# Performance work log

Measured on AMD Instinct MI355X. Metric: run time of the kernel, lower is better.

The kernel has to match this reference:

```python
import jax, jax.numpy as jnp
import numpy as np

B, S, D, H, E, K = 4, 1024, 1024, 4096, 8, 2


def setup_inputs() -> dict:
    key = jax.random.key(0)
    k1, k2, k3, k4 = jax.random.split(key, 4)
    x = jax.random.normal(k1, (B, S, D), dtype=jnp.float32)
    # expert params: two-layer MLP per expert, stacked along expert axis
    W1 = jax.random.normal(k2, (E, D, H), dtype=jnp.float32) * 0.02
    b1 = jnp.zeros((E, H), dtype=jnp.float32)
    W2 = jax.random.normal(k3, (E, H, D), dtype=jnp.float32) * 0.02
    b2 = jnp.zeros((E, D), dtype=jnp.float32)
    # hash-router assignments: k expert ids per token (stands in for HashRouter output)
    assign = jax.random.randint(k4, (B, S, K), 0, E, dtype=jnp.int64)
    return {"x": x, "W1": W1, "b1": b1, "W2": W2, "b2": b2, "assign": assign, "k": K}


def reference(x, W1, b1, W2, b2, assign, k):
    E_ = W1.shape[0]
    # mask[b,s,e] = 1 if expert e appears in assign[b,s,:] (matches (assign==idx).any(-1),
    # so a duplicated assignment contributes once, exactly like the torch loop)
    mask = (assign[..., None] == jnp.arange(E_)[None, None, None, :]).any(axis=-2)
    # run every token through every expert, then mask-combine (dense MoE reference)
    h = jax.nn.relu(jnp.einsum('bsd,edh->bseh', x, W1) + b1)      # [B,S,E,H]
    y = jnp.einsum('bseh,ehd->bsed', h, W2) + b2                  # [B,S,E,D]
    out = jnp.einsum('bsed,bse->bsd', y, mask.astype(x.dtype))
    return out / k
```

## Files before the change

kernel.cpp:

```cpp
#include <hip/hip_runtime.h>
#include <hip/hip_bf16.h>

#define DIM_D 1024
#define DIM_H 4096
#define NUM_E 8
#define NUM_TOK 4096
#define MAXROWS 8320

typedef __attribute__((ext_vector_type(8))) short short8;
typedef __attribute__((ext_vector_type(4))) float floatx4;

__device__ __forceinline__ unsigned short f2bf(float f) {
  union { float f; unsigned int u; } v; v.f = f;
  unsigned int r = v.u + 0x7fffu + ((v.u >> 16) & 1u);
  return (unsigned short)(r >> 16);
}

__device__ __forceinline__ void async_copy16(const void* g, void* l) {
  __builtin_amdgcn_global_load_lds(
      (__attribute__((address_space(1))) unsigned int*)(g),
      (__attribute__((address_space(3))) unsigned int*)(l), 16, 0, 0);
}


__global__ void route_count(const int* __restrict__ assign, int* __restrict__ counts) {
  int t = blockIdx.x * blockDim.x + threadIdx.x;
  if (t < NUM_TOK) {
    int e0 = assign[2 * t], e1 = assign[2 * t + 1];
    atomicAdd(&counts[e0], 1);
    if (e1 != e0) atomicAdd(&counts[e1], 1);
  }
}

__global__ void scan_k(const int* __restrict__ counts, int* __restrict__ offsets,
                       int* __restrict__ cursors) {
  if (threadIdx.x == 0 && blockIdx.x == 0) {
    int acc = 0;
    for (int e = 0; e < NUM_E; e++) {
      offsets[e] = acc; cursors[e] = acc; acc += counts[e];
    }
  }
}

__global__ void gather_k(const float* __restrict__ x, const int* __restrict__ assign,
                         int* __restrict__ cursors, int* __restrict__ tok2row,
                         unsigned short* __restrict__ Xg) {
  int t = blockIdx.x;
  __shared__ int sr[2];
  if (threadIdx.x == 0) {
    int e0 = assign[2 * t], e1 = assign[2 * t + 1];
    int r0 = atomicAdd(&cursors[e0], 1);
    int r1 = (e1 != e0) ? atomicAdd(&cursors[e1], 1) : -1;
    tok2row[2 * t] = r0; tok2row[2 * t + 1] = r1;
    sr[0] = r0; sr[1] = r1;
  }
  __syncthreads();
  int r0 = sr[0], r1 = sr[1];
  const float4* xv = (const float4*)(x + (size_t)t * DIM_D);
  float4 v0 = xv[threadIdx.x * 2];
  float4 v1 = xv[threadIdx.x * 2 + 1];
  unsigned short h[8];
  h[0] = f2bf(v0.x); h[1] = f2bf(v0.y); h[2] = f2bf(v0.z); h[3] = f2bf(v0.w);
  h[4] = f2bf(v1.x); h[5] = f2bf(v1.y); h[6] = f2bf(v1.z); h[7] = f2bf(v1.w);
  uint4 pack = *(uint4*)h;
  *(uint4*)(Xg + (size_t)r0 * DIM_D + threadIdx.x * 8) = pack;
  if (r1 >= 0)
    *(uint4*)(Xg + (size_t)r1 * DIM_D + threadIdx.x * 8) = pack;
}

__global__ void transpose_cvt(const float* __restrict__ in, unsigned short* __restrict__ outp,
                              int R, int C) {
  __shared__ float tile[64][65];
  int e = blockIdx.z;
  const float* ip = in + (size_t)e * R * C + (size_t)(blockIdx.y * 64) * C + blockIdx.x * 64;
  unsigned short* op = outp + (size_t)e * R * C + (size_t)(blockIdx.x * 64) * R + blockIdx.y * 64;
  int rr = threadIdx.x >> 4;
  int c4 = (threadIdx.x & 15) * 4;
#pragma unroll
  for (int i = 0; i < 4; i++) {
    int r = rr + i * 16;
    float4 v = *(const float4*)(ip + (size_t)r * C + c4);
    tile[r][c4 + 0] = v.x; tile[r][c4 + 1] = v.y;
    tile[r][c4 + 2] = v.z; tile[r][c4 + 3] = v.w;
  }
  __syncthreads();
  int r8 = (threadIdx.x & 7) * 8;
  int cbase = threadIdx.x >> 3;
#pragma unroll
  for (int it = 0; it < 2; it++) {
    int c = cbase + it * 32;
    unsigned short h[8];
#pragma unroll
    for (int j = 0; j < 8; j++) h[j] = f2bf(tile[r8 + j][c]);
    *(uint4*)(op + (size_t)c * R + r8) = *(const uint4*)h;
  }
}

template <int MODE>
__global__ __launch_bounds__(256) void moe_gemm(
    const unsigned short* __restrict__ A, const unsigned short* __restrict__ Bt,
    const float* __restrict__ bias, const int* __restrict__ counts,
    const int* __restrict__ offsets,
    unsigned short* __restrict__ Hout, float* __restrict__ Yout,
    int K, int N) {
  const int e = blockIdx.z;
  const int cnt = counts[e];
  int mt_, nt_;
  if (MODE == 0) {
    nt_ = (blockIdx.x & 7) | ((blockIdx.y & 3) << 3);
    mt_ = (blockIdx.x >> 3) | ((blockIdx.y >> 2) << 2);
  } else {
    nt_ = blockIdx.x; mt_ = blockIdx.y;
  }
  const int m0 = mt_ * 128;
  if (m0 >= cnt) return;
  const int n0 = nt_ * 128;
  const int rowbase = offsets[e];

  __shared__ unsigned short sh[2 * 128 * 64];
  unsigned short* As = sh;
  unsigned short* Bs = sh + 128 * 64;

  const int tid = threadIdx.x;
  const int w = tid >> 6;
  const int lane = tid & 63;
  const int l15 = lane & 15, l4 = lane >> 4;
  const int wm = w >> 1, wn = w & 1;
  const int lrow = lane >> 3, lslot = lane & 7;
  const int lchunk = lslot ^ lrow;

  const unsigned short* gA[4]; const unsigned short* gB[4];
  void* dA[4]; void* dB[4];
  const unsigned short* Bbase = Bt + (size_t)e * N * K;
#pragma unroll
  for (int p = 0; p < 4; p++) {
    int rw = p * 32 + w * 8;
    gA[p] = A + (size_t)(rowbase + m0 + rw + lrow) * K + lchunk * 8;
    gB[p] = Bbase + (size_t)(n0 + rw + lrow) * K + lchunk * 8;
    dA[p] = (char*)As + rw * 128;
    dB[p] = (char*)Bs + rw * 128;
  }

  floatx4 acc[4][4];
#pragma unroll
  for (int i = 0; i < 4; i++)
#pragma unroll
    for (int j = 0; j < 4; j++) acc[i][j] = (floatx4){0.f, 0.f, 0.f, 0.f};

  int arow[4], brow[4], sl[2];
  sl[0] = ((l4 + 0) ^ (l15 & 7)) * 8;
  sl[1] = ((l4 + 4) ^ (l15 & 7)) * 8;
#pragma unroll
  for (int mt = 0; mt < 4; mt++) arow[mt] = (wm * 64 + mt * 16 + l15) * 64;
#pragma unroll
  for (int nt = 0; nt < 4; nt++) brow[nt] = (wn * 64 + nt * 16 + l15) * 64;

  for (int k0 = 0; k0 < K; k0 += 64) {
    __syncthreads();
#pragma unroll
    for (int p = 0; p < 4; p++) async_copy16(gA[p], dA[p]);
#pragma unroll
    for (int p = 0; p < 4; p++) async_copy16(gB[p], dB[p]);
#pragma unroll
    for (int p = 0; p < 4; p++) { gA[p] += 64; gB[p] += 64; }
    __syncthreads();
#pragma unroll
    for (int s = 0; s < 2; s++) {
      short8 a[4], b[4];
#pragma unroll
      for (int mt = 0; mt < 4; mt++) a[mt] = *(const short8*)(As + arow[mt] + sl[s]);
#pragma unroll
      for (int nt = 0; nt < 4; nt++) b[nt] = *(const short8*)(Bs + brow[nt] + sl[s]);
#pragma unroll
      for (int mt = 0; mt < 4; mt++)
#pragma unroll
        for (int nt = 0; nt < 4; nt++)
          acc[mt][nt] = __builtin_amdgcn_mfma_f32_16x16x32_bf16(a[mt], b[nt], acc[mt][nt], 0, 0, 0);
    }
  }

  __syncthreads();
  float* sbuf = (float*)sh + w * 1088;
  const float* be = bias + (size_t)e * N + n0 + wn * 64;
#pragma unroll
  for (int mt = 0; mt < 4; mt++) {
#pragma unroll
    for (int nt = 0; nt < 4; nt++) {
      float bv = be[nt * 16 + l15];
#pragma unroll
      for (int r = 0; r < 4; r++) {
        float v = acc[mt][nt][r] + bv;
        if (MODE == 0) v = fmaxf(v, 0.f);
        sbuf[(l4 * 4 + r) * 68 + nt * 16 + l15] = v;
      }
    }
    __syncthreads();
#pragma unroll
    for (int pass = 0; pass < 4; pass++) {
      int row = pass * 4 + l4;
      int col4 = l15 * 4;
      int gm = m0 + wm * 64 + mt * 16 + row;
      float4 v = *(const float4*)&sbuf[row * 68 + col4];
      if (gm < cnt) {
        size_t off = (size_t)(rowbase + gm) * N + n0 + wn * 64 + col4;
        if (MODE == 0) {
          ushort4 h;
          h.x = f2bf(v.x); h.y = f2bf(v.y); h.z = f2bf(v.z); h.w = f2bf(v.w);
          *(ushort4*)(Hout + off) = h;
        } else {
          *(float4*)(Yout + off) = v;
        }
      }
    }
    __syncthreads();
  }
}

__global__ void combine_k(const float* __restrict__ Yg, const int* __restrict__ tok2row,
                          const int* __restrict__ kptr, float* __restrict__ out) {
  int t = blockIdx.x;
  int r0 = tok2row[2 * t], r1 = tok2row[2 * t + 1];
  float invk = 1.0f / (float)kptr[0];
  int d = threadIdx.x * 4;
  float4 v = *(const float4*)(Yg + (size_t)r0 * DIM_D + d);
  if (r1 >= 0) {
    float4 u = *(const float4*)(Yg + (size_t)r1 * DIM_D + d);
    v.x += u.x; v.y += u.y; v.z += u.z; v.w += u.w;
  }
  float4 o; o.x = v.x * invk; o.y = v.y * invk; o.z = v.z * invk; o.w = v.w * invk;
  *(float4*)(out + (size_t)t * DIM_D + d) = o;
}


extern "C" void kernel_launch(void* const* d_in, const int* in_sizes, int n_in,
                              void* d_out, int out_size, void* d_ws, size_t ws_size,
                              hipStream_t stream) {
  const float* x = (const float*)d_in[0];
  const float* W1 = (const float*)d_in[1];
  const float* b1 = (const float*)d_in[2];
  const float* W2 = (const float*)d_in[3];
  const float* b2 = (const float*)d_in[4];
  const int* assign = (const int*)d_in[5];
  const int* kptr = (const int*)d_in[6];
  float* out = (float*)d_out;

  char* p = (char*)d_ws;
  int* counts = (int*)p; p += 256;
  int* offsets = (int*)p; p += 256;
  int* cursors = (int*)p; p += 256;
  int* tok2row = (int*)p; p += NUM_TOK * 2 * 4;
  unsigned short* Xg = (unsigned short*)p; p += (size_t)MAXROWS * DIM_D * 2;
  unsigned short* Hg = (unsigned short*)p; p += (size_t)MAXROWS * DIM_H * 2;
  unsigned short* W1t = (unsigned short*)p; p += (size_t)NUM_E * DIM_D * DIM_H * 2;
  unsigned short* W2t = (unsigned short*)p; p += (size_t)NUM_E * DIM_D * DIM_H * 2;
  float* Yg = (float*)W1t;

  hipMemsetAsync(counts, 0, 256, stream);

  route_count<<<(NUM_TOK + 255) / 256, 256, 0, stream>>>(assign, counts);
  scan_k<<<1, 64, 0, stream>>>(counts, offsets, cursors);
  gather_k<<<NUM_TOK, 128, 0, stream>>>(x, assign, cursors, tok2row, Xg);

  transpose_cvt<<<dim3(DIM_H / 64, DIM_D / 64, NUM_E), 256, 0, stream>>>(W1, W1t, DIM_D, DIM_H);
  transpose_cvt<<<dim3(DIM_D / 64, DIM_H / 64, NUM_E), 256, 0, stream>>>(W2, W2t, DIM_H, DIM_D);

  moe_gemm<0><<<dim3(DIM_H / 128, 32, NUM_E), 256, 0, stream>>>(
      Xg, W1t, b1, counts, offsets, Hg, nullptr, DIM_D, DIM_H);
  moe_gemm<1><<<dim3(DIM_D / 128, 32, NUM_E), 256, 0, stream>>>(
      Hg, W2t, b2, counts, offsets, nullptr, Yg, DIM_H, DIM_D);

  combine_k<<<NUM_TOK, 256, 0, stream>>>(Yg, tok2row, kptr, out);
}
```

Before: 656.2 us.

## Split-K second GEMM, merge routing kernels, fuse weight transposes, drop epilogue barriers

Merges the count and scan kernels into one single-block LDS histogram kernel, which also removes the memset. The two weight transpose/convert launches become one launch with 128x32 tiles. The second GEMM is split along K into two halves, writing separate fp32 partial planes that the combine kernel sums, so twice as many blocks can fill the GPU. The per-wave epilogue replaces __syncthreads with lgkmcnt waits, since each wave uses its own staging buffer. The workspace is reordered so the two Y planes fit in the region that held W1t.

Result: faster. 634.2 us (-3.4%).

```diff
diff --git a/kernel.cpp b/kernel.cpp
--- a/kernel.cpp
+++ b/kernel.cpp
@@ -23,21 +23,22 @@
 }
 
 
-__global__ void route_count(const int* __restrict__ assign, int* __restrict__ counts) {
-  int t = blockIdx.x * blockDim.x + threadIdx.x;
-  if (t < NUM_TOK) {
+__global__ void route_scan(const int* __restrict__ assign, int* __restrict__ counts,
+                           int* __restrict__ offsets, int* __restrict__ cursors) {
+  __shared__ int hist[NUM_E];
+  int tid = threadIdx.x;
+  if (tid < NUM_E) hist[tid] = 0;
+  __syncthreads();
+  for (int t = tid; t < NUM_TOK; t += 256) {
     int e0 = assign[2 * t], e1 = assign[2 * t + 1];
-    atomicAdd(&counts[e0], 1);
-    if (e1 != e0) atomicAdd(&counts[e1], 1);
-  }
-}
-
-__global__ void scan_k(const int* __restrict__ counts, int* __restrict__ offsets,
-                       int* __restrict__ cursors) {
-  if (threadIdx.x == 0 && blockIdx.x == 0) {
+    atomicAdd(&hist[e0], 1);
+    if (e1 != e0) atomicAdd(&hist[e1], 1);
+  }
+  __syncthreads();
+  if (tid == 0) {
     int acc = 0;
     for (int e = 0; e < NUM_E; e++) {
-      offsets[e] = acc; cursors[e] = acc; acc += counts[e];
+      counts[e] = hist[e]; offsets[e] = acc; cursors[e] = acc; acc += hist[e];
     }
   }
 }
@@ -68,42 +69,53 @@
     *(uint4*)(Xg + (size_t)r1 * DIM_D + threadIdx.x * 8) = pack;
 }
 
-__global__ void transpose_cvt(const float* __restrict__ in, unsigned short* __restrict__ outp,
-                              int R, int C) {
-  __shared__ float tile[64][65];
-  int e = blockIdx.z;
-  const float* ip = in + (size_t)e * R * C + (size_t)(blockIdx.y * 64) * C + blockIdx.x * 64;
-  unsigned short* op = outp + (size_t)e * R * C + (size_t)(blockIdx.x * 64) * R + blockIdx.y * 64;
-  int rr = threadIdx.x >> 4;
-  int c4 = (threadIdx.x & 15) * 4;
-#pragma unroll
-  for (int i = 0; i < 4; i++) {
-    int r = rr + i * 16;
-    float4 v = *(const float4*)(ip + (size_t)r * C + c4);
+__global__ __launch_bounds__(256) void transpose_cvt2(
+    const float* __restrict__ W1, const float* __restrict__ W2,
+    unsigned short* __restrict__ W1t, unsigned short* __restrict__ W2t) {
+  __shared__ float tile[128][33];
+  const int z = blockIdx.y;
+  const int e = z >> 1, which = z & 1;
+  const int R = which ? DIM_H : DIM_D;
+  const int C = which ? DIM_D : DIM_H;
+  const int nbx = C / 32;
+  const int bx = blockIdx.x % nbx;
+  const int by = blockIdx.x / nbx;
+  const float* ip = (which ? W2 : W1) + (size_t)e * R * C;
+  unsigned short* op = (which ? W2t : W1t) + (size_t)e * R * C;
+  const int tid = threadIdx.x;
+
+  int rr = tid >> 3;
+  int c4 = (tid & 7) * 4;
+#pragma unroll
+  for (int p = 0; p < 4; p++) {
+    int r = p * 32 + rr;
+    float4 v = *(const float4*)(ip + (size_t)(by * 128 + r) * C + bx * 32 + c4);
     tile[r][c4 + 0] = v.x; tile[r][c4 + 1] = v.y;
     tile[r][c4 + 2] = v.z; tile[r][c4 + 3] = v.w;
   }
   __syncthreads();
-  int r8 = (threadIdx.x & 7) * 8;
-  int cbase = threadIdx.x >> 3;
-#pragma unroll
-  for (int it = 0; it < 2; it++) {
-    int c = cbase + it * 32;
+  int cc = tid >> 4;
+  int r8 = (tid & 15) * 8;
+#pragma unroll
+  for (int q = 0; q < 2; q++) {
+    int c = q * 16 + cc;
     unsigned short h[8];
 #pragma unroll
     for (int j = 0; j < 8; j++) h[j] = f2bf(tile[r8 + j][c]);
-    *(uint4*)(op + (size_t)c * R + r8) = *(const uint4*)h;
-  }
-}
-
-template <int MODE>
+    *(uint4*)(op + (size_t)(bx * 32 + c) * R + by * 128 + r8) = *(const uint4*)h;
+  }
+}
+
+template <int MODE, int KTOT>
 __global__ __launch_bounds__(256) void moe_gemm(
-    const unsigned short* __restrict__ A, const unsigned short* __restrict__ Bt,
+    const unsigned short* __restrict__ Ain, const unsigned short* __restrict__ Bt,
     const float* __restrict__ bias, const int* __restrict__ counts,
     const int* __restrict__ offsets,
     unsigned short* __restrict__ Hout, float* __restrict__ Yout,
-    int K, int N) {
-  const int e = blockIdx.z;
+    int lda, int ldb, int N) {
+  int e, half;
+  if (MODE == 0) { e = blockIdx.z; half = 0; }
+  else           { e = blockIdx.z >> 1; half = blockIdx.z & 1; }
   const int cnt = counts[e];
   int mt_, nt_;
   if (MODE == 0) {
@@ -116,6 +128,7 @@
   if (m0 >= cnt) return;
   const int n0 = nt_ * 128;
   const int rowbase = offsets[e];
+  const unsigned short* A = Ain + (size_t)half * KTOT;
 
   __shared__ unsigned short sh[2 * 128 * 64];
   unsigned short* As = sh;
@@ -131,12 +144,12 @@
 
   const unsigned short* gA[4]; const unsigned short* gB[4];
   void* dA[4]; void* dB[4];
-  const unsigned short* Bbase = Bt + (size_t)e * N * K;
+  const unsigned short* Bbase = Bt + (size_t)e * N * ldb + (size_t)half * KTOT;
 #pragma unroll
   for (int p = 0; p < 4; p++) {
     int rw = p * 32 + w * 8;
-    gA[p] = A + (size_t)(rowbase + m0 + rw + lrow) * K + lchunk * 8;
-    gB[p] = Bbase + (size_t)(n0 + rw + lrow) * K + lchunk * 8;
+    gA[p] = A + (size_t)(rowbase + m0 + rw + lrow) * lda + lchunk * 8;
+    gB[p] = Bbase + (size_t)(n0 + rw + lrow) * ldb + lchunk * 8;
     dA[p] = (char*)As + rw * 128;
     dB[p] = (char*)Bs + rw * 128;
   }
@@ -155,7 +168,7 @@
 #pragma unroll
   for (int nt = 0; nt < 4; nt++) brow[nt] = (wn * 64 + nt * 16 + l15) * 64;
 
-  for (int k0 = 0; k0 < K; k0 += 64) {
+  for (int k0 = 0; k0 < KTOT; k0 += 64) {
     __syncthreads();
 #pragma unroll
     for (int p = 0; p < 4; p++) async_copy16(gA[p], dA[p]);
@@ -181,12 +194,14 @@
 
   __syncthreads();
   float* sbuf = (float*)sh + w * 1088;
+  const bool addb = (MODE == 0) || (half == 0);
   const float* be = bias + (size_t)e * N + n0 + wn * 64;
+  float* yplane = (MODE == 1) ? (Yout + (size_t)half * MAXROWS * N) : nullptr;
 #pragma unroll
   for (int mt = 0; mt < 4; mt++) {
 #pragma unroll
     for (int nt = 0; nt < 4; nt++) {
-      float bv = be[nt * 16 + l15];
+      float bv = addb ? be[nt * 16 + l15] : 0.f;
 #pragma unroll
       for (int r = 0; r < 4; r++) {
         float v = acc[mt][nt][r] + bv;
@@ -194,7 +209,7 @@
         sbuf[(l4 * 4 + r) * 68 + nt * 16 + l15] = v;
       }
     }
-    __syncthreads();
+    __asm__ __volatile__("s_waitcnt lgkmcnt(0)" ::: "memory");
 #pragma unroll
     for (int pass = 0; pass < 4; pass++) {
       int row = pass * 4 + l4;
@@ -208,11 +223,11 @@
           h.x = f2bf(v.x); h.y = f2bf(v.y); h.z = f2bf(v.z); h.w = f2bf(v.w);
           *(ushort4*)(Hout + off) = h;
         } else {
-          *(float4*)(Yout + off) = v;
+          *(float4*)(yplane + off) = v;
         }
       }
     }
-    __syncthreads();
+    __asm__ __volatile__("s_waitcnt lgkmcnt(0)" ::: "memory");
   }
 }
 
@@ -222,10 +237,14 @@
   int r0 = tok2row[2 * t], r1 = tok2row[2 * t + 1];
   float invk = 1.0f / (float)kptr[0];
   int d = threadIdx.x * 4;
+  const size_t plane = (size_t)MAXROWS * DIM_D;
   float4 v = *(const float4*)(Yg + (size_t)r0 * DIM_D + d);
+  float4 u = *(const float4*)(Yg + plane + (size_t)r0 * DIM_D + d);
+  v.x += u.x; v.y += u.y; v.z += u.z; v.w += u.w;
   if (r1 >= 0) {
-    float4 u = *(const float4*)(Yg + (size_t)r1 * DIM_D + d);
-    v.x += u.x; v.y += u.y; v.z += u.z; v.w += u.w;
+    float4 a = *(const float4*)(Yg + (size_t)r1 * DIM_D + d);
+    float4 b = *(const float4*)(Yg + plane + (size_t)r1 * DIM_D + d);
+    v.x += a.x + b.x; v.y += a.y + b.y; v.z += a.z + b.z; v.w += a.w + b.w;
   }
   float4 o; o.x = v.x * invk; o.y = v.y * invk; o.z = v.z * invk; o.w = v.w * invk;
   *(float4*)(out + (size_t)t * DIM_D + d) = o;
@@ -249,25 +268,21 @@
   int* offsets = (int*)p; p += 256;
   int* cursors = (int*)p; p += 256;
   int* tok2row = (int*)p; p += NUM_TOK * 2 * 4;
+  unsigned short* W1t = (unsigned short*)p; p += (size_t)NUM_E * DIM_D * DIM_H * 2;
   unsigned short* Xg = (unsigned short*)p; p += (size_t)MAXROWS * DIM_D * 2;
   unsigned short* Hg = (unsigned short*)p; p += (size_t)MAXROWS * DIM_H * 2;
-  unsigned short* W1t = (unsigned short*)p; p += (size_t)NUM_E * DIM_D * DIM_H * 2;
   unsigned short* W2t = (unsigned short*)p; p += (size_t)NUM_E * DIM_D * DIM_H * 2;
   float* Yg = (float*)W1t;
 
-  hipMemsetAsync(counts, 0, 256, stream);
-
-  route_count<<<(NUM_TOK + 255) / 256, 256, 0, stream>>>(assign, counts);
-  scan_k<<<1, 64, 0, stream>>>(counts, offsets, cursors);
+  route_scan<<<1, 256, 0, stream>>>(assign, counts, offsets, cursors);
   gather_k<<<NUM_TOK, 128, 0, stream>>>(x, assign, cursors, tok2row, Xg);
 
-  transpose_cvt<<<dim3(DIM_H / 64, DIM_D / 64, NUM_E), 256, 0, stream>>>(W1, W1t, DIM_D, DIM_H);
-  transpose_cvt<<<dim3(DIM_D / 64, DIM_H / 64, NUM_E), 256, 0, stream>>>(W2, W2t, DIM_H, DIM_D);
-
-  moe_gemm<0><<<dim3(DIM_H / 128, 32, NUM_E), 256, 0, stream>>>(
-      Xg, W1t, b1, counts, offsets, Hg, nullptr, DIM_D, DIM_H);
-  moe_gemm<1><<<dim3(DIM_D / 128, 32, NUM_E), 256, 0, stream>>>(
-      Hg, W2t, b2, counts, offsets, nullptr, Yg, DIM_H, DIM_D);
+  transpose_cvt2<<<dim3(1024, 16), 256, 0, stream>>>(W1, W2, W1t, W2t);
+
+  moe_gemm<0, DIM_D><<<dim3(32, 32, NUM_E), 256, 0, stream>>>(
+      Xg, W1t, b1, counts, offsets, Hg, nullptr, DIM_D, DIM_D, DIM_H);
+  moe_gemm<1, DIM_H / 2><<<dim3(8, 32, NUM_E * 2), 256, 0, stream>>>(
+      Hg, W2t, b2, counts, offsets, nullptr, Yg, DIM_H, DIM_H, DIM_D);
 
   combine_k<<<NUM_TOK, 256, 0, stream>>>(Yg, tok2row, kptr, out);
 }
```
